# Performance work log

Measured on AMD Instinct MI355X. Metric: run time of the kernel, lower is better.

The kernel has to match this reference:

```python
import jax, jax.numpy as jnp
import numpy as np

B, C, H, W = 32, 1536, 24, 24
HID, D, K = 512, 128, 64  # hidden, cluster_dim, num_clusters


def setup_inputs() -> dict:
    key = jax.random.key(0)
    ks = jax.random.split(key, 6)
    def rn(k, shape, scale):
        return jax.random.normal(k, shape, dtype=jnp.float32) * scale
    return {
        "x": rn(ks[0], (B, C, H, W), 1.0),
        # cluster_features: Conv2d(C,512,1) -> ReLU -> Conv2d(512,D,1)
        "w1c": rn(ks[1], (HID, C), 0.02), "b1c": jnp.zeros((HID,), jnp.float32),
        "w2c": rn(ks[2], (D, HID), 0.02), "b2c": jnp.zeros((D,), jnp.float32),
        # score: Conv2d(C,512,1) -> ReLU -> Conv2d(512,K,1)
        "w1s": rn(ks[3], (HID, C), 0.02), "b1s": jnp.zeros((HID,), jnp.float32),
        "w2s": rn(ks[4], (K, HID), 0.02), "b2s": jnp.zeros((K,), jnp.float32),
        "temperature": jnp.array(1.0, jnp.float32),
    }


def _sinkhorn_log(S, num_iters=3):
    # log-domain OT solver with uniform marginals log(1/n), reg=1 (M/reg == M)
    b, m, n = S.shape
    norm = -jnp.log(jnp.asarray(n, S.dtype))
    log_a = jnp.full((b, m), norm, S.dtype)
    log_b = jnp.full((b, n), norm, S.dtype)
    u = jnp.zeros((b, m), S.dtype)
    v = jnp.zeros((b, n), S.dtype)
    for _ in range(num_iters):
        u = log_a - jax.nn.logsumexp(S + v[:, None, :], axis=2)
        v = log_b - jax.nn.logsumexp(S + u[:, :, None], axis=1)
    # get_matching_probs subtracts norm at the end
    return S + u[:, :, None] + v[:, None, :] - norm


def reference(x, w1c, b1c, w2c, b2c, w1s, b1s, w2s, b2s, temperature):
    b, c, h, w = x.shape
    xf = x.reshape(b, c, h * w)  # (B, C, N); 1x1 conv == channel GEMM
    # cluster features f: (B, D, N)
    hc = jax.nn.relu(jnp.einsum('oc,bcn->bon', w1c, xf) + b1c[None, :, None])
    f = jnp.einsum('oc,bcn->bon', w2c, hc) + b2c[None, :, None]
    # assignment scores p: (B, K, N)
    hs = jax.nn.relu(jnp.einsum('oc,bcn->bon', w1s, xf) + b1s[None, :, None])
    s = jnp.einsum('oc,bcn->bon', w2s, hs) + b2s[None, :, None]
    log_p = _sinkhorn_log(s, num_iters=3)
    p = jnp.exp(log_p / temperature) + jnp.exp(log_p)  # (B, K, N)
    # (f.unsqueeze(2) * p.unsqueeze(1)).sum(-1) == batched matmul
    agg = jnp.einsum('bcn,bkn->bck', f, p)  # (B, D, K)
    flat = agg.reshape(b, -1)
    nrm = jnp.maximum(jnp.linalg.norm(flat, axis=-1, keepdims=True), 1e-12)
    return flat / nrm
```

## Files before the change

### kernel.cpp

```cpp
#include <hip/hip_runtime.h>

typedef unsigned short ushort_t;
typedef float f32x4 __attribute__((ext_vector_type(4)));
typedef short short8 __attribute__((ext_vector_type(8)));

#define B_   32
#define C_   1536
#define N_   576
#define HID_ 512
#define D_   128
#define K_   64

__device__ __forceinline__ float bf2f(ushort_t u) {
    union { unsigned u; float f; } c; c.u = ((unsigned)u) << 16; return c.f;
}
__device__ __forceinline__ ushort_t f2bf(float x) {
    unsigned u = __float_as_uint(x);
    return (ushort_t)((u + 0x7FFFu + ((u >> 16) & 1u)) >> 16);
}

typedef const __attribute__((address_space(1))) char gas_char;
typedef __attribute__((address_space(3))) char las_char;
__device__ __forceinline__ void cp16(const void* g, void* l) {
    __builtin_amdgcn_global_load_lds((gas_char*)(size_t)g,
                                     (las_char*)(unsigned)(size_t)l, 16, 0, 0);
}
__device__ __forceinline__ void bar() {
    asm volatile("" ::: "memory");
    __builtin_amdgcn_s_barrier();
    asm volatile("" ::: "memory");
}

#define OB1_  1572864
#define OW2C_ 1573888
#define OB2C_ 1639424
#define OW2S_ 1639552
#define OB2S_ 1672320
#define WTOT_ 1672384
#define TRB_  6912
#define CVB4_ (((WTOT_ / 4) + 255) / 256)

__global__ __launch_bounds__(256) void prep_kernel(
    const void* __restrict__ x,
    const void* __restrict__ w1c, const void* __restrict__ b1c,
    const void* __restrict__ w2c, const void* __restrict__ b2c,
    const void* __restrict__ w1s, const void* __restrict__ b1s,
    const void* __restrict__ w2s, const void* __restrict__ b2s,
    const unsigned* __restrict__ temp,
    ushort_t* __restrict__ xt, ushort_t* __restrict__ o, float* __restrict__ Tp)
{
    __shared__ ushort_t t[64][68];
    unsigned d = temp[0];
    int flag = (d == 0x3F800000u) ? 1 : 0;
    int tid = threadIdx.x;
    int idx = blockIdx.x;
    if (idx == 0 && tid == 0)
        *Tp = flag ? __uint_as_float(d) : bf2f((ushort_t)(d & 0xFFFFu));

    if (idx < TRB_) {
        int b = idx / 216, rem = idx % 216;
        int c0 = (rem % 24) * 64, n0 = (rem / 24) * 64;
        ushort_t* xtb = xt + (size_t)b * N_ * C_;
        int r = tid >> 4, c4 = (tid & 15) * 4;
        if (flag) {
            const float* xb = (const float*)x + (size_t)b * C_ * N_;
#pragma unroll
            for (int i = 0; i < 4; ++i) {
                int cc = r + i * 16;
                float4 v = *(const float4*)&xb[(size_t)(c0 + cc) * N_ + n0 + c4];
                t[cc][c4 + 0] = f2bf(v.x);
                t[cc][c4 + 1] = f2bf(v.y);
                t[cc][c4 + 2] = f2bf(v.z);
                t[cc][c4 + 3] = f2bf(v.w);
            }
        } else {
            const ushort_t* xb = (const ushort_t*)x + (size_t)b * C_ * N_;
#pragma unroll
            for (int i = 0; i < 4; ++i) {
                int cc = r + i * 16;
                *(uint2*)&t[cc][c4] =
                    *(const uint2*)&xb[(size_t)(c0 + cc) * N_ + n0 + c4];
            }
        }
        __syncthreads();
#pragma unroll
        for (int i = 0; i < 4; ++i) {
            int nn = r + i * 16;
            ushort_t v0 = t[c4 + 0][nn], v1 = t[c4 + 1][nn];
            ushort_t v2 = t[c4 + 2][nn], v3 = t[c4 + 3][nn];
            uint2 vv;
            vv.x = (unsigned)v0 | ((unsigned)v1 << 16);
            vv.y = (unsigned)v2 | ((unsigned)v3 << 16);
            *(uint2*)&xtb[(size_t)(n0 + nn) * C_ + c0 + c4] = vv;
        }
    } else {
        int i4 = ((idx - TRB_) * 256 + tid) * 4;
        if (i4 >= WTOT_) return;
        const void* p; int off;
        if      (i4 < 786432)  { p = w1c; off = i4; }
        else if (i4 < OB1_)    { p = w1s; off = i4 - 786432; }
        else if (i4 < 1573376) { p = b1c; off = i4 - OB1_; }
        else if (i4 < OW2C_)   { p = b1s; off = i4 - 1573376; }
        else if (i4 < OB2C_)   { p = w2c; off = i4 - OW2C_; }
        else if (i4 < OW2S_)   { p = b2c; off = i4 - OB2C_; }
        else if (i4 < OB2S_)   { p = w2s; off = i4 - OW2S_; }
        else                   { p = b2s; off = i4 - OB2S_; }
        if (flag) {
            float4 v = *(const float4*)((const float*)p + off);
            uint2 r;
            r.x = (unsigned)f2bf(v.x) | ((unsigned)f2bf(v.y) << 16);
            r.y = (unsigned)f2bf(v.z) | ((unsigned)f2bf(v.w) << 16);
            *(uint2*)&o[i4] = r;
        } else {
            *(uint2*)&o[i4] = *(const uint2*)((const ushort_t*)p + off);
        }
    }
}

__global__ __launch_bounds__(256) void gemm1_kernel(
    const ushort_t* __restrict__ Xt, const ushort_t* __restrict__ W1,
    const ushort_t* __restrict__ bias, ushort_t* __restrict__ h)
{
    __shared__ ushort_t Atile[2][128 * 64];
    __shared__ ushort_t Btile[2][128 * 64];
    int idx = blockIdx.x;
    int l = (idx & 7) * 144 + (idx >> 3);
    int mt = l >> 3, t = l & 7;
    int row0 = mt * 128, col0 = t * 128;

    int tid = threadIdx.x, w = tid >> 6, lane = tid & 63;
    int wr = w >> 1, wc = w & 1;
    int r16 = lane & 15, q = lane >> 4, kh = q * 8;

    int srow = tid >> 3;
    int cx = ((tid & 7) ^ (srow & 7)) * 8;
    const ushort_t* ag[4];
    const ushort_t* bg[4];
#pragma unroll
    for (int s = 0; s < 4; ++s) {
        ag[s] = Xt + (size_t)(row0 + s * 32 + srow) * C_ + cx;
        bg[s] = W1 + (size_t)(col0 + s * 32 + srow) * C_ + cx;
    }

    f32x4 acc[4][4];
#pragma unroll
    for (int i = 0; i < 4; ++i)
#pragma unroll
        for (int j = 0; j < 4; ++j) acc[i][j] = f32x4{0.f, 0.f, 0.f, 0.f};

    int rowa = wr * 64 + r16;
    int rowb = wc * 64 + r16;
    int xr = (r16 & 7) * 8;

    auto stage = [&](int buf) {
#pragma unroll
        for (int s = 0; s < 4; ++s) {
            cp16(ag[s], &Atile[buf][tid * 8 + s * 2048]);
            cp16(bg[s], &Btile[buf][tid * 8 + s * 2048]);
            ag[s] += 64; bg[s] += 64;
        }
    };
    auto compute = [&](int cb) {
#pragma unroll
        for (int ks = 0; ks < 2; ++ks) {
            int ke = (ks * 32 + kh) ^ xr;
            short8 af[4], bf[4];
#pragma unroll
            for (int i = 0; i < 4; ++i)
                af[i] = *(const short8*)&Atile[cb][(rowa + i * 16) * 64 + ke];
#pragma unroll
            for (int j = 0; j < 4; ++j)
                bf[j] = *(const short8*)&Btile[cb][(rowb + j * 16) * 64 + ke];
#pragma unroll
            for (int i = 0; i < 4; ++i)
#pragma unroll
                for (int j = 0; j < 4; ++j)
                    acc[i][j] = __builtin_amdgcn_mfma_f32_16x16x32_bf16(
                        af[i], bf[j], acc[i][j], 0, 0, 0);
        }
    };

    stage(0);
    int cur = 0;
    for (int kt = 0; kt < 23; ++kt) {
        stage(cur ^ 1);
        asm volatile("s_waitcnt vmcnt(8)" ::: "memory");
        bar();
        compute(cur);
        bar();
        cur ^= 1;
    }
    asm volatile("s_waitcnt vmcnt(0)" ::: "memory");
    bar();
    compute(cur);

#pragma unroll
    for (int j = 0; j < 4; ++j) {
        int col = col0 + wc * 64 + j * 16 + r16;
        float cb = bf2f(bias[col]);
#pragma unroll
        for (int i = 0; i < 4; ++i) {
            int rowo = row0 + wr * 64 + i * 16 + q * 4;
#pragma unroll
            for (int r = 0; r < 4; ++r) {
                float v = fmaxf(acc[i][j][r] + cb, 0.f);
                h[(size_t)(rowo + r) * 1024 + col] = f2bf(v);
            }
        }
    }
}

__global__ __launch_bounds__(256) void gemm2_kernel(
    const ushort_t* __restrict__ Wb, const ushort_t* __restrict__ h,
    ushort_t* __restrict__ fbuf, float* __restrict__ sbuf)
{
    __shared__ ushort_t Atile[2][128 * 32];
    __shared__ ushort_t Btile[2][128 * 32];
    int nt = blockIdx.x, b = blockIdx.y, z = blockIdx.z;
    int col0 = nt * 128;
    int Mclamp = z ? K_ : D_;
    const ushort_t* Aw   = Wb + (z ? OW2S_ : OW2C_);
    const ushort_t* bias = Wb + (z ? OB2S_ : OB2C_);
    const ushort_t* hb = h + (size_t)b * N_ * 1024 + (z ? 512 : 0);

    int tid = threadIdx.x, w = tid >> 6, lane = tid & 63;
    int wr = w >> 1, wc = w & 1;
    int r16 = lane & 15, q = lane >> 4, kh = q * 8;

    int srow = tid >> 2;
    int swz = ((tid & 3) ^ (srow & 3)) * 8;
    int ar0 = min(srow, Mclamp - 1);
    int ar1 = min(64 + srow, Mclamp - 1);
    const ushort_t* ag0 = Aw + (size_t)ar0 * HID_ + swz;
    const ushort_t* ag1 = Aw + (size_t)ar1 * HID_ + swz;
    int br0 = min(col0 + srow, N_ - 1);
    int br1 = min(col0 + 64 + srow, N_ - 1);
    const ushort_t* bg0 = hb + (size_t)br0 * 1024 + swz;
    const ushort_t* bg1 = hb + (size_t)br1 * 1024 + swz;

    f32x4 acc[4][4];
#pragma unroll
    for (int i = 0; i < 4; ++i)
#pragma unroll
        for (int j = 0; j < 4; ++j) acc[i][j] = f32x4{0.f, 0.f, 0.f, 0.f};

    int xr = (r16 & 3) * 8;

    auto stage = [&](int buf) {
        cp16(ag0, &Atile[buf][tid * 8]);
        cp16(ag1, &Atile[buf][2048 + tid * 8]);
        cp16(bg0, &Btile[buf][tid * 8]);
        cp16(bg1, &Btile[buf][2048 + tid * 8]);
        ag0 += 32; ag1 += 32; bg0 += 32; bg1 += 32;
    };
    auto compute = [&](int cb) {
        int ke = kh ^ xr;
        short8 af[4], bf[4];
#pragma unroll
        for (int i = 0; i < 4; ++i)
            af[i] = *(const short8*)&Atile[cb][(wr * 64 + i * 16 + r16) * 32 + ke];
#pragma unroll
        for (int j = 0; j < 4; ++j)
            bf[j] = *(const short8*)&Btile[cb][(wc * 64 + j * 16 + r16) * 32 + ke];
#pragma unroll
        for (int i = 0; i < 4; ++i)
#pragma unroll
            for (int j = 0; j < 4; ++j)
                acc[i][j] = __builtin_amdgcn_mfma_f32_16x16x32_bf16(
                    af[i], bf[j], acc[i][j], 0, 0, 0);
    };

    stage(0);
    int cur = 0;
    for (int kt = 0; kt < 15; ++kt) {
        stage(cur ^ 1);
        asm volatile("s_waitcnt vmcnt(4)" ::: "memory");
        bar();
        compute(cur);
        bar();
        cur ^= 1;
    }
    asm volatile("s_waitcnt vmcnt(0)" ::: "memory");
    bar();
    compute(cur);

#pragma unroll
    for (int j = 0; j < 4; ++j) {
        int col = col0 + wc * 64 + j * 16 + r16;
#pragma unroll
        for (int i = 0; i < 4; ++i) {
            int rowb = wr * 64 + i * 16 + q * 4;
#pragma unroll
            for (int r = 0; r < 4; ++r) {
                int rr = rowb + r;
                if (rr < Mclamp && col < N_) {
                    float v = acc[i][j][r] + bf2f(bias[rr]);
                    if (z == 0)
                        fbuf[(size_t)b * D_ * N_ + (size_t)rr * N_ + col] = f2bf(v);
                    else
                        sbuf[(size_t)b * K_ * N_ + (size_t)rr * N_ + col] = v;
                }
            }
        }
    }
}

__global__ __launch_bounds__(512) void sinkhorn_kernel(
    const float* __restrict__ s_all, float* __restrict__ uv)
{
    int b = blockIdx.x;
    const float* S = s_all + (size_t)b * K_ * N_;
    __shared__ float su[K_];
    __shared__ float sv[N_];
    int tid = threadIdx.x, w = tid >> 6, lane = tid & 63;
    const float norm = -logf((float)N_);

    for (int n = tid; n < N_; n += 512) sv[n] = 0.f;
    __syncthreads();

    for (int it = 0; it < 3; ++it) {
        for (int r = w; r < K_; r += 8) {
            const float* Sr = S + r * N_;
            float a0 = 0.f, a1 = 0.f, a2 = 0.f;
#pragma unroll
            for (int k = 0; k < 9; k += 3) {
                int n0 = lane + 64 * k;
                a0 += __expf(Sr[n0] + sv[n0]);
                a1 += __expf(Sr[n0 + 64] + sv[n0 + 64]);
                a2 += __expf(Sr[n0 + 128] + sv[n0 + 128]);
            }
            float t = a0 + a1 + a2;
#pragma unroll
            for (int off = 32; off; off >>= 1) t += __shfl_xor(t, off);
            if (lane == 0) su[r] = norm - __logf(t);
        }
        __syncthreads();
        for (int n = tid; n < N_; n += 512) {
            const float* Sc = S + n;
            float a0 = 0.f, a1 = 0.f, a2 = 0.f, a3 = 0.f;
#pragma unroll
            for (int m = 0; m < K_; m += 4) {
                a0 += __expf(Sc[(m + 0) * N_] + su[m + 0]);
                a1 += __expf(Sc[(m + 1) * N_] + su[m + 1]);
                a2 += __expf(Sc[(m + 2) * N_] + su[m + 2]);
                a3 += __expf(Sc[(m + 3) * N_] + su[m + 3]);
            }
            sv[n] = norm - __logf((a0 + a1) + (a2 + a3));
        }
        __syncthreads();
    }
    float* ub = uv + (size_t)b * 640;
    if (tid < K_) ub[tid] = su[tid];
    for (int n = tid; n < N_; n += 512) ub[64 + n] = sv[n];
}

__global__ __launch_bounds__(256) void agg_kernel(
    const ushort_t* __restrict__ f_all, const float* __restrict__ s_all,
    const float* __restrict__ uv, const float* __restrict__ Tp,
    float* __restrict__ aggws)
{
    int rblk = blockIdx.x;
    int b = blockIdx.y;
    const float* S = s_all + (size_t)b * K_ * N_;
    __shared__ float su[K_];
    __shared__ float sv[N_];
    __shared__ ushort_t Ftile[16 * 32];
    __shared__ ushort_t Ptile[64 * 32];
    int tid = threadIdx.x, w = tid >> 6, lane = tid & 63;
    int r16 = lane & 15, q = lane >> 4;
    const float norm = -logf((float)N_);
    const float* ub = uv + (size_t)b * 640;
    if (tid < K_) su[tid] = ub[tid];
    for (int n = tid; n < N_; n += 256) sv[n] = ub[64 + n];
    __syncthreads();

    float invT = 1.f / (*Tp);
    const ushort_t* f = f_all + (size_t)b * D_ * N_ + (size_t)(rblk * 16) * N_;
    int frow = tid >> 2, fch = tid & 3;
    const ushort_t* fg = f + (size_t)frow * N_ + (size_t)((fch ^ (frow & 3)) * 8);
    int prow = tid >> 2, pc0 = (tid & 3) * 8;
    int pswz = ((tid & 3) ^ (prow & 3)) * 8;
    float urow = su[prow];
    const float* Srow = S + (size_t)prow * N_ + pc0;
    int xa = (q ^ (r16 & 3)) * 8;

    f32x4 acc = f32x4{0.f, 0.f, 0.f, 0.f};

    for (int s = 0; s < 18; ++s) {
        if (tid < 64) cp16(fg, &Ftile[tid * 8]);
        fg += 32;
        int nb = s * 32;
        ushort_t pv[8];
#pragma unroll
        for (int e = 0; e < 8; ++e) {
            float lp = Srow[e] + urow + sv[nb + pc0 + e] - norm;
            pv[e] = f2bf(__expf(lp * invT) + __expf(lp));
        }
        Srow += 32;
        uint2 w0, w1;
        w0.x = (unsigned)pv[0] | ((unsigned)pv[1] << 16);
        w0.y = (unsigned)pv[2] | ((unsigned)pv[3] << 16);
        w1.x = (unsigned)pv[4] | ((unsigned)pv[5] << 16);
        w1.y = (unsigned)pv[6] | ((unsigned)pv[7] << 16);
        *(uint2*)&Ptile[prow * 32 + pswz] = w0;
        *(uint2*)&Ptile[prow * 32 + pswz + 4] = w1;
        __syncthreads();
        short8 af = *(const short8*)&Ftile[r16 * 32 + xa];
        short8 bf = *(const short8*)&Ptile[(w * 16 + r16) * 32 + xa];
        acc = __builtin_amdgcn_mfma_f32_16x16x32_bf16(af, bf, acc, 0, 0, 0);
        __syncthreads();
    }
    float* ao = aggws + (size_t)b * (D_ * K_) + (size_t)(rblk * 16) * K_ + (w * 16 + r16);
#pragma unroll
    for (int r = 0; r < 4; ++r)
        ao[(size_t)(q * 4 + r) * K_] = acc[r];
}

__global__ __launch_bounds__(256) void norm_kernel(
    const float* __restrict__ aggws, const unsigned* __restrict__ temp,
    void* __restrict__ out)
{
    int b = blockIdx.x, tid = threadIdx.x, w = tid >> 6, lane = tid & 63;
    __shared__ float red[4];
    const float4* a4 = (const float4*)(aggws + (size_t)b * (D_ * K_));
    float4 v[8];
    float ssq = 0.f;
#pragma unroll
    for (int i = 0; i < 8; ++i) {
        v[i] = a4[tid + i * 256];
        ssq += v[i].x * v[i].x + v[i].y * v[i].y + v[i].z * v[i].z + v[i].w * v[i].w;
    }
#pragma unroll
    for (int off = 32; off; off >>= 1) ssq += __shfl_xor(ssq, off);
    if (lane == 0) red[w] = ssq;
    __syncthreads();
    float tot = red[0] + red[1] + red[2] + red[3];
    float inv = 1.f / fmaxf(sqrtf(tot), 1e-12f);
    int flag = (temp[0] == 0x3F800000u) ? 1 : 0;
    if (flag) {
        float4* o4 = (float4*)out + (size_t)b * 2048;
#pragma unroll
        for (int i = 0; i < 8; ++i) {
            float4 t = v[i];
            t.x *= inv; t.y *= inv; t.z *= inv; t.w *= inv;
            o4[tid + i * 256] = t;
        }
    } else {
        ushort_t* ob = (ushort_t*)out + (size_t)b * 8192;
#pragma unroll
        for (int i = 0; i < 8; ++i) {
            uint2 p;
            p.x = (unsigned)f2bf(v[i].x * inv) | ((unsigned)f2bf(v[i].y * inv) << 16);
            p.y = (unsigned)f2bf(v[i].z * inv) | ((unsigned)f2bf(v[i].w * inv) << 16);
            *(uint2*)&ob[(size_t)(tid + i * 256) * 4] = p;
        }
    }
}

extern "C" void kernel_launch(void* const* d_in, const int* in_sizes, int n_in,
                              void* d_out, int out_size, void* d_ws, size_t ws_size,
                              hipStream_t stream) {
    const void* x    = d_in[0];
    const void* w1c  = d_in[1];
    const void* b1c  = d_in[2];
    const void* w2c  = d_in[3];
    const void* b2c  = d_in[4];
    const void* w1s  = d_in[5];
    const void* b1s  = d_in[6];
    const void* w2s  = d_in[7];
    const void* b2s  = d_in[8];
    const unsigned* temp = (const unsigned*)d_in[9];

    char* ws = (char*)d_ws;
    float* Tp = (float*)ws;
    ushort_t* Wb = (ushort_t*)(ws + 256);
    size_t offXt = 256 + (((size_t)WTOT_ * 2 + 255) & ~(size_t)255);
    ushort_t* Xt = (ushort_t*)(ws + offXt);
    size_t xtBytes = (size_t)B_ * N_ * C_ * 2;
    size_t hBytes  = (size_t)B_ * N_ * 1024 * 2;
    ushort_t* h  = (ushort_t*)(ws + offXt + xtBytes);
    size_t o0 = offXt;
    ushort_t* fbuf = (ushort_t*)(ws + o0);  o0 += (size_t)B_ * D_ * N_ * 2;
    float*    sbuf = (float*)(ws + o0);     o0 += (size_t)B_ * K_ * N_ * 4;
    float* uvws  = (float*)(ws + offXt + xtBytes + hBytes);
    float* aggws = uvws + (size_t)B_ * 640;

    prep_kernel<<<dim3(TRB_ + CVB4_), 256, 0, stream>>>(
        x, w1c, b1c, w2c, b2c, w1s, b1s, w2s, b2s, temp, Xt, Wb, Tp);
    gemm1_kernel<<<dim3(1152), 256, 0, stream>>>(Xt, Wb, Wb + OB1_, h);
    gemm2_kernel<<<dim3(5, B_, 2), 256, 0, stream>>>(Wb, h, fbuf, sbuf);
    sinkhorn_kernel<<<dim3(B_), 512, 0, stream>>>(sbuf, uvws);
    agg_kernel<<<dim3(8, B_), 256, 0, stream>>>(fbuf, sbuf, uvws, Tp, aggws);
    norm_kernel<<<dim3(B_), 256, 0, stream>>>(aggws, temp, (void*)d_out);
}
```

Baseline: 314.7 us.

## Stage scores in LDS for Sinkhorn, emit P there, fuse aggregation with normalization

The Sinkhorn kernel now loads each batch's score matrix into padded shared memory once, instead of re-reading global memory on every row and column pass. It also computes the bf16 assignment matrix P at the end and writes it out. The separate aggregation and norm kernels are merged into one kernel per batch that does a double-buffered 128x64 MFMA GEMM over P and f, then L2-normalizes in registers. This removes one launch, the fp32 agg round trip, and the recomputation of exp in the aggregation step. In exchange, only 32 blocks run the aggregation, and the Sinkhorn kernel needs about 150KB of LDS.

```diff
diff --git a/kernel.cpp b/kernel.cpp
--- a/kernel.cpp
+++ b/kernel.cpp
@@ -306,21 +306,32 @@
 }
 
 __global__ __launch_bounds__(512) void sinkhorn_kernel(
-    const float* __restrict__ s_all, float* __restrict__ uv)
+    const float* __restrict__ s_all, const float* __restrict__ Tp,
+    ushort_t* __restrict__ P_all)
 {
     int b = blockIdx.x;
     const float* S = s_all + (size_t)b * K_ * N_;
+    __shared__ float Sl[K_ * 577];
     __shared__ float su[K_];
     __shared__ float sv[N_];
     int tid = threadIdx.x, w = tid >> 6, lane = tid & 63;
     const float norm = -logf((float)N_);
 
+    const float4* S4 = (const float4*)S;
+    for (int g = tid; g < (K_ * N_) / 4; g += 512) {
+        float4 v = S4[g];
+        int w0 = g * 4;
+        int r = w0 / N_;
+        int base = w0 + r;
+        Sl[base + 0] = v.x; Sl[base + 1] = v.y;
+        Sl[base + 2] = v.z; Sl[base + 3] = v.w;
+    }
     for (int n = tid; n < N_; n += 512) sv[n] = 0.f;
     __syncthreads();
 
     for (int it = 0; it < 3; ++it) {
         for (int r = w; r < K_; r += 8) {
-            const float* Sr = S + r * N_;
+            const float* Sr = Sl + r * 577;
             float a0 = 0.f, a1 = 0.f, a2 = 0.f;
 #pragma unroll
             for (int k = 0; k < 9; k += 3) {
@@ -336,100 +347,122 @@
         }
         __syncthreads();
         for (int n = tid; n < N_; n += 512) {
-            const float* Sc = S + n;
+            const float* Sc = Sl + n;
             float a0 = 0.f, a1 = 0.f, a2 = 0.f, a3 = 0.f;
 #pragma unroll
             for (int m = 0; m < K_; m += 4) {
-                a0 += __expf(Sc[(m + 0) * N_] + su[m + 0]);
-                a1 += __expf(Sc[(m + 1) * N_] + su[m + 1]);
-                a2 += __expf(Sc[(m + 2) * N_] + su[m + 2]);
-                a3 += __expf(Sc[(m + 3) * N_] + su[m + 3]);
+                a0 += __expf(Sc[(m + 0) * 577] + su[m + 0]);
+                a1 += __expf(Sc[(m + 1) * 577] + su[m + 1]);
+                a2 += __expf(Sc[(m + 2) * 577] + su[m + 2]);
+                a3 += __expf(Sc[(m + 3) * 577] + su[m + 3]);
             }
             sv[n] = norm - __logf((a0 + a1) + (a2 + a3));
         }
         __syncthreads();
     }
-    float* ub = uv + (size_t)b * 640;
-    if (tid < K_) ub[tid] = su[tid];
-    for (int n = tid; n < N_; n += 512) ub[64 + n] = sv[n];
-}
-
-__global__ __launch_bounds__(256) void agg_kernel(
-    const ushort_t* __restrict__ f_all, const float* __restrict__ s_all,
-    const float* __restrict__ uv, const float* __restrict__ Tp,
-    float* __restrict__ aggws)
+
+    float invT = 1.f / (*Tp);
+    ushort_t* Pb = P_all + (size_t)b * K_ * N_;
+    for (int r = w; r < K_; r += 8) {
+        float ur = su[r];
+        const float* Sr = Sl + r * 577;
+#pragma unroll
+        for (int k = 0; k < 9; ++k) {
+            int n0 = lane + 64 * k;
+            float lp = Sr[n0] + ur + sv[n0] - norm;
+            Pb[r * N_ + n0] = f2bf(__expf(lp * invT) + __expf(lp));
+        }
+    }
+}
+
+__global__ __launch_bounds__(256) void aggnorm_kernel(
+    const ushort_t* __restrict__ f_all, const ushort_t* __restrict__ P_all,
+    const unsigned* __restrict__ temp, void* __restrict__ out)
 {
-    int rblk = blockIdx.x;
-    int b = blockIdx.y;
-    const float* S = s_all + (size_t)b * K_ * N_;
-    __shared__ float su[K_];
-    __shared__ float sv[N_];
-    __shared__ ushort_t Ftile[16 * 32];
-    __shared__ ushort_t Ptile[64 * 32];
+    __shared__ ushort_t Atile[2][128 * 64];
+    __shared__ ushort_t Ptile[2][64 * 64];
+    __shared__ float red[4];
+    int b = blockIdx.x;
+    const ushort_t* F = f_all + (size_t)b * D_ * N_;
+    const ushort_t* P = P_all + (size_t)b * K_ * N_;
     int tid = threadIdx.x, w = tid >> 6, lane = tid & 63;
-    int r16 = lane & 15, q = lane >> 4;
-    const float norm = -logf((float)N_);
-    const float* ub = uv + (size_t)b * 640;
-    if (tid < K_) su[tid] = ub[tid];
-    for (int n = tid; n < N_; n += 256) sv[n] = ub[64 + n];
-    __syncthreads();
-
-    float invT = 1.f / (*Tp);
-    const ushort_t* f = f_all + (size_t)b * D_ * N_ + (size_t)(rblk * 16) * N_;
-    int frow = tid >> 2, fch = tid & 3;
-    const ushort_t* fg = f + (size_t)frow * N_ + (size_t)((fch ^ (frow & 3)) * 8);
-    int prow = tid >> 2, pc0 = (tid & 3) * 8;
-    int pswz = ((tid & 3) ^ (prow & 3)) * 8;
-    float urow = su[prow];
-    const float* Srow = S + (size_t)prow * N_ + pc0;
-    int xa = (q ^ (r16 & 3)) * 8;
-
-    f32x4 acc = f32x4{0.f, 0.f, 0.f, 0.f};
-
-    for (int s = 0; s < 18; ++s) {
-        if (tid < 64) cp16(fg, &Ftile[tid * 8]);
-        fg += 32;
-        int nb = s * 32;
-        ushort_t pv[8];
-#pragma unroll
-        for (int e = 0; e < 8; ++e) {
-            float lp = Srow[e] + urow + sv[nb + pc0 + e] - norm;
-            pv[e] = f2bf(__expf(lp * invT) + __expf(lp));
-        }
-        Srow += 32;
-        uint2 w0, w1;
-        w0.x = (unsigned)pv[0] | ((unsigned)pv[1] << 16);
-        w0.y = (unsigned)pv[2] | ((unsigned)pv[3] << 16);
-        w1.x = (unsigned)pv[4] | ((unsigned)pv[5] << 16);
-        w1.y = (unsigned)pv[6] | ((unsigned)pv[7] << 16);
-        *(uint2*)&Ptile[prow * 32 + pswz] = w0;
-        *(uint2*)&Ptile[prow * 32 + pswz + 4] = w1;
-        __syncthreads();
-        short8 af = *(const short8*)&Ftile[r16 * 32 + xa];
-        short8 bf = *(const short8*)&Ptile[(w * 16 + r16) * 32 + xa];
-        acc = __builtin_amdgcn_mfma_f32_16x16x32_bf16(af, bf, acc, 0, 0, 0);
-        __syncthreads();
-    }
-    float* ao = aggws + (size_t)b * (D_ * K_) + (size_t)(rblk * 16) * K_ + (w * 16 + r16);
-#pragma unroll
-    for (int r = 0; r < 4; ++r)
-        ao[(size_t)(q * 4 + r) * K_] = acc[r];
-}
-
-__global__ __launch_bounds__(256) void norm_kernel(
-    const float* __restrict__ aggws, const unsigned* __restrict__ temp,
-    void* __restrict__ out)
-{
-    int b = blockIdx.x, tid = threadIdx.x, w = tid >> 6, lane = tid & 63;
-    __shared__ float red[4];
-    const float4* a4 = (const float4*)(aggws + (size_t)b * (D_ * K_));
-    float4 v[8];
+    int wr = w >> 1, wc = w & 1;
+    int r16 = lane & 15, q = lane >> 4, kh = q * 8;
+
+    int srow = tid >> 3;
+    int cx = ((tid & 7) ^ (srow & 7)) * 8;
+    const ushort_t* fg[4];
+    const ushort_t* pg[2];
+#pragma unroll
+    for (int s = 0; s < 4; ++s)
+        fg[s] = F + (size_t)(s * 32 + srow) * N_ + cx;
+#pragma unroll
+    for (int s = 0; s < 2; ++s)
+        pg[s] = P + (size_t)(s * 32 + srow) * N_ + cx;
+
+    f32x4 acc[4][2];
+#pragma unroll
+    for (int i = 0; i < 4; ++i)
+#pragma unroll
+        for (int j = 0; j < 2; ++j) acc[i][j] = f32x4{0.f, 0.f, 0.f, 0.f};
+
+    int rowa = wr * 64 + r16;
+    int rowp = wc * 32 + r16;
+    int xr = (r16 & 7) * 8;
+
+    auto stage = [&](int buf) {
+#pragma unroll
+        for (int s = 0; s < 4; ++s) {
+            cp16(fg[s], &Atile[buf][tid * 8 + s * 2048]);
+            fg[s] += 64;
+        }
+#pragma unroll
+        for (int s = 0; s < 2; ++s) {
+            cp16(pg[s], &Ptile[buf][tid * 8 + s * 2048]);
+            pg[s] += 64;
+        }
+    };
+    auto compute = [&](int cb) {
+#pragma unroll
+        for (int ks = 0; ks < 2; ++ks) {
+            int ke = (ks * 32 + kh) ^ xr;
+            short8 af[4], pf[2];
+#pragma unroll
+            for (int i = 0; i < 4; ++i)
+                af[i] = *(const short8*)&Atile[cb][(rowa + i * 16) * 64 + ke];
+#pragma unroll
+            for (int j = 0; j < 2; ++j)
+                pf[j] = *(const short8*)&Ptile[cb][(rowp + j * 16) * 64 + ke];
+#pragma unroll
+            for (int i = 0; i < 4; ++i)
+#pragma unroll
+                for (int j = 0; j < 2; ++j)
+                    acc[i][j] = __builtin_amdgcn_mfma_f32_16x16x32_bf16(
+                        af[i], pf[j], acc[i][j], 0, 0, 0);
+        }
+    };
+
+    stage(0);
+    int cur = 0;
+    for (int kt = 0; kt < 8; ++kt) {
+        stage(cur ^ 1);
+        asm volatile("s_waitcnt vmcnt(6)" ::: "memory");
+        bar();
+        compute(cur);
+        bar();
+        cur ^= 1;
+    }
+    asm volatile("s_waitcnt vmcnt(0)" ::: "memory");
+    bar();
+    compute(cur);
+
     float ssq = 0.f;
 #pragma unroll
-    for (int i = 0; i < 8; ++i) {
-        v[i] = a4[tid + i * 256];
-        ssq += v[i].x * v[i].x + v[i].y * v[i].y + v[i].z * v[i].z + v[i].w * v[i].w;
-    }
+    for (int i = 0; i < 4; ++i)
+#pragma unroll
+        for (int j = 0; j < 2; ++j)
+#pragma unroll
+            for (int r = 0; r < 4; ++r) { float v = acc[i][j][r]; ssq += v * v; }
 #pragma unroll
     for (int off = 32; off; off >>= 1) ssq += __shfl_xor(ssq, off);
     if (lane == 0) red[w] = ssq;
@@ -437,22 +470,19 @@
     float tot = red[0] + red[1] + red[2] + red[3];
     float inv = 1.f / fmaxf(sqrtf(tot), 1e-12f);
     int flag = (temp[0] == 0x3F800000u) ? 1 : 0;
-    if (flag) {
-        float4* o4 = (float4*)out + (size_t)b * 2048;
-#pragma unroll
-        for (int i = 0; i < 8; ++i) {
-            float4 t = v[i];
-            t.x *= inv; t.y *= inv; t.z *= inv; t.w *= inv;
-            o4[tid + i * 256] = t;
-        }
-    } else {
-        ushort_t* ob = (ushort_t*)out + (size_t)b * 8192;
-#pragma unroll
-        for (int i = 0; i < 8; ++i) {
-            uint2 p;
-            p.x = (unsigned)f2bf(v[i].x * inv) | ((unsigned)f2bf(v[i].y * inv) << 16);
-            p.y = (unsigned)f2bf(v[i].z * inv) | ((unsigned)f2bf(v[i].w * inv) << 16);
-            *(uint2*)&ob[(size_t)(tid + i * 256) * 4] = p;
+#pragma unroll
+    for (int i = 0; i < 4; ++i) {
+#pragma unroll
+        for (int j = 0; j < 2; ++j) {
+            int col = wc * 32 + j * 16 + r16;
+#pragma unroll
+            for (int r = 0; r < 4; ++r) {
+                int row = wr * 64 + i * 16 + q * 4 + r;
+                float v = acc[i][j][r] * inv;
+                size_t idx = (size_t)b * D_ * K_ + (size_t)row * K_ + col;
+                if (flag) ((float*)out)[idx] = v;
+                else      ((ushort_t*)out)[idx] = f2bf(v);
+            }
         }
     }
 }
@@ -477,19 +507,16 @@
     size_t offXt = 256 + (((size_t)WTOT_ * 2 + 255) & ~(size_t)255);
     ushort_t* Xt = (ushort_t*)(ws + offXt);
     size_t xtBytes = (size_t)B_ * N_ * C_ * 2;
-    size_t hBytes  = (size_t)B_ * N_ * 1024 * 2;
     ushort_t* h  = (ushort_t*)(ws + offXt + xtBytes);
     size_t o0 = offXt;
     ushort_t* fbuf = (ushort_t*)(ws + o0);  o0 += (size_t)B_ * D_ * N_ * 2;
     float*    sbuf = (float*)(ws + o0);     o0 += (size_t)B_ * K_ * N_ * 4;
-    float* uvws  = (float*)(ws + offXt + xtBytes + hBytes);
-    float* aggws = uvws + (size_t)B_ * 640;
+    ushort_t* Pws  = (ushort_t*)(ws + o0);  o0 += (size_t)B_ * K_ * N_ * 2;
 
     prep_kernel<<<dim3(TRB_ + CVB4_), 256, 0, stream>>>(
         x, w1c, b1c, w2c, b2c, w1s, b1s, w2s, b2s, temp, Xt, Wb, Tp);
     gemm1_kernel<<<dim3(1152), 256, 0, stream>>>(Xt, Wb, Wb + OB1_, h);
     gemm2_kernel<<<dim3(5, B_, 2), 256, 0, stream>>>(Wb, h, fbuf, sbuf);
-    sinkhorn_kernel<<<dim3(B_), 512, 0, stream>>>(sbuf, uvws);
-    agg_kernel<<<dim3(8, B_), 256, 0, stream>>>(fbuf, sbuf, uvws, Tp, aggws);
-    norm_kernel<<<dim3(B_), 256, 0, stream>>>(aggws, temp, (void*)d_out);
-}
+    sinkhorn_kernel<<<dim3(B_), 512, 0, stream>>>(sbuf, Tp, Pws);
+    aggnorm_kernel<<<dim3(B_), 256, 0, stream>>>(fbuf, Pws, temp, (void*)d_out);
+}
```

New measurement: 310.3 us. Within noise of the previous version (-1.4%).
